# Kernel optimization log

Measured on AMD Instinct MI355X. Metric: run time of the kernel, lower is better.

The kernel has to match this reference:

```python
import jax, jax.numpy as jnp
import numpy as np

NSUB = 4  # fixed RK4 substeps per save interval (replaces diffrax adaptive stepping)


def _mlp(x, W0, b0, Wh, bh, Wo, bo, act, fact):
    h = act(W0 @ x + b0)
    for k in range(Wh.shape[0]):  # 3 stacked middle layers (static)
        h = act(Wh[k] @ h + bh[k])
    return fact(Wo @ h + bo)


def _forward(ts, ys, iW0, ib0, iWh, ibh, iWo, ibo, fW0, fb0, fWh, fbh, fWo, fbo, lW, lb):
    hid = iWo.shape[0]
    C = iW0.shape[1]  # in_size + 1 control channels

    def single(yseq):  # yseq: (T, obs)
        tys = jnp.concatenate([ts[:, None], yseq], axis=-1)  # (T, C)
        dts = ts[1:] - ts[:-1]                                # (T-1,)
        diffs = (tys[1:] - tys[:-1]) / dts[:, None]           # (T-1, C)
        # backward Hermite: deriv at t_i is backward difference, forward diff at t_0
        deriv = jnp.concatenate([diffs[:1], diffs], axis=0)   # (T, C)
        d0 = deriv[:-1]
        d1 = deriv[1:]
        c = (3.0 * diffs - 2.0 * d0 - d1) / dts[:, None]
        b = (d0 + d1 - 2.0 * diffs) / (dts * dts)[:, None]

        y0 = _mlp(tys[0], iW0, ib0, iWh, ibh, iWo, ibo, jax.nn.relu, lambda z: z)

        def vf(y):  # (hid, C)
            return _mlp(y, fW0, fb0, fWh, fbh, fWo, fbo, jax.nn.softplus, jnp.tanh).reshape(hid, C)

        def interval(y, xs):
            d0i, ci, bi, h = xs
            hs = h / NSUB

            def xdot(s):  # derivative of cubic Hermite control at local time s
                return d0i + 2.0 * ci * s + 3.0 * bi * s * s

            def f(s, yy):
                return vf(yy) @ xdot(s)

            def sub(k, yy):  # one RK4 substep
                s = k * hs
                k1 = f(s, yy)
                k2 = f(s + hs / 2, yy + hs / 2 * k1)
                k3 = f(s + hs / 2, yy + hs / 2 * k2)
                k4 = f(s + hs, yy + hs * k3)
                return yy + hs / 6 * (k1 + 2 * k2 + 2 * k3 + k4)

            y = jax.lax.fori_loop(0, NSUB, sub, y)
            return y, y

        _, ytail = jax.lax.scan(interval, y0, (d0, c, b, dts))
        ysol = jnp.concatenate([y0[None], ytail], axis=0)  # (T, hid)
        return ysol @ lW.T + lb                            # evolving_out readout

    return jax.vmap(single)(ys)


def setup_inputs() -> dict:
    key = jax.random.key(0)
    ks = jax.random.split(key, 10)
    T, B, obs, hid, width, out_size = 128, 64, 32, 64, 128, 32
    C = obs + 1
    fout = hid * C

    def lin(k, o, i):
        return jax.random.normal(k, (o, i), jnp.float32) / np.sqrt(i).astype(np.float32)

    return {
        "ts": jnp.arange(T, dtype=jnp.float32) / T,
        "ys": jax.random.normal(ks[0], (B, T, obs), jnp.float32) * 0.1,
        "iW0": lin(ks[1], width, C), "ib0": jnp.zeros((width,), jnp.float32),
        "iWh": jax.random.normal(ks[2], (3, width, width), jnp.float32) / np.sqrt(width).astype(np.float32),
        "ibh": jnp.zeros((3, width), jnp.float32),
        "iWo": lin(ks[3], hid, width), "ibo": jnp.zeros((hid,), jnp.float32),
        "fW0": lin(ks[4], width, hid), "fb0": jnp.zeros((width,), jnp.float32),
        "fWh": jax.random.normal(ks[5], (3, width, width), jnp.float32) / np.sqrt(width).astype(np.float32),
        "fbh": jnp.zeros((3, width), jnp.float32),
        "fWo": lin(ks[6], fout, width), "fbo": jnp.zeros((fout,), jnp.float32),
        "lW": lin(ks[7], out_size, hid), "lb": jnp.zeros((out_size,), jnp.float32),
    }


def reference(ts, ys, iW0, ib0, iWh, ibh, iWo, ibo, fW0, fb0, fWh, fbh, fWo, fbo, lW, lb):
    return _forward(ts, ys, iW0, ib0, iWh, ibh, iWo, ibo, fW0, fb0, fWh, fbh, fWo, fbo, lW, lb)
```

## Files before the change

kernel.cpp:

```cpp
#include <hip/hip_runtime.h>
#include <stdint.h>

#define T_N   128
#define B_N   64
#define OBS   32
#define C_N   33
#define HID   64
#define WID   128
#define FOUT  2112
#define OUTD  32
#define NSUB  4
#define NTH   1024

#define NTILE_T  132
#define NPLANES  (NTILE_T*4)
#define WS_NEED  ((size_t)NPLANES * 64 * 16)

typedef __attribute__((ext_vector_type(8))) short  bf16x8;
typedef __attribute__((ext_vector_type(4))) float  f32x4;

__device__ __forceinline__ float b2f(unsigned short u) {
    return __uint_as_float(((unsigned int)u) << 16);
}
__device__ __forceinline__ float b2f_lo(unsigned int u) {
    return __uint_as_float(u << 16);
}
__device__ __forceinline__ float b2f_hi(unsigned int u) {
    return __uint_as_float(u & 0xffff0000u);
}
__device__ __forceinline__ unsigned short f2b(float f) {
    unsigned int u = __float_as_uint(f);
    unsigned int lsb = (u >> 16) & 1u;
    u += 0x7fffu + lsb;
    return (unsigned short)(u >> 16);
}
__device__ __forceinline__ unsigned int pack2(float a, float b) {
    return ((unsigned int)f2b(a)) | (((unsigned int)f2b(b)) << 16);
}
__device__ __forceinline__ unsigned int pkhi(float a, float b) {
    return (__float_as_uint(a) >> 16) | (__float_as_uint(b) & 0xffff0000u);
}
__device__ __forceinline__ unsigned int pklo(float a, float b) {
    float la = a - __uint_as_float(__float_as_uint(a) & 0xffff0000u);
    float lb = b - __uint_as_float(__float_as_uint(b) & 0xffff0000u);
    return pack2(la, lb);
}
__device__ __forceinline__ bf16x8 u4b8(uint4 u) {
    union { uint4 a; bf16x8 b; } x; x.a = u; return x.b;
}
__device__ __forceinline__ float softplus_f(float x) {
    return fmaxf(x, 0.f) + __logf(1.f + __expf(-fabsf(x)));
}
__device__ __forceinline__ float tanh_fast(float x) {
    float e = __expf(2.f * x);
    return 1.f - 2.f / (e + 1.f);
}

struct PolBF16 {
    static __device__ __forceinline__ float ld(const void* p, int i) {
        return b2f(((const unsigned short*)p)[i]);
    }
    static __device__ __forceinline__ void ld8(const void* p, int i, float* o) {
        uint4 u = *(const uint4*)((const unsigned short*)p + i);
        o[0]=b2f_lo(u.x); o[1]=b2f_hi(u.x); o[2]=b2f_lo(u.y); o[3]=b2f_hi(u.y);
        o[4]=b2f_lo(u.z); o[5]=b2f_hi(u.z); o[6]=b2f_lo(u.w); o[7]=b2f_hi(u.w);
    }
    static __device__ __forceinline__ void st(void* p, int i, float v) {
        ((unsigned short*)p)[i] = f2b(v);
    }
};
struct PolF32 {
    static __device__ __forceinline__ float ld(const void* p, int i) {
        return ((const float*)p)[i];
    }
    static __device__ __forceinline__ void ld8(const void* p, int i, float* o) {
        const float4* q = (const float4*)((const float*)p + i);
        float4 a = q[0], b = q[1];
        o[0]=a.x; o[1]=a.y; o[2]=a.z; o[3]=a.w;
        o[4]=b.x; o[5]=b.y; o[6]=b.z; o[7]=b.w;
    }
    static __device__ __forceinline__ void st(void* p, int i, float v) {
        ((float*)p)[i] = v;
    }
};

struct __align__(16) Smem {
    uint4 whf[3][32][64];
    uint4 w0f[16][64];
    float rowp[2][FOUT];
    unsigned int hpk[2][2][64];
    unsigned int ypk[2][32];
    float y[HID];
    float yt[HID];
    float xd[C_N], d0[C_N], cc[C_N], bb[C_N];
    float fb0[WID];
    float fbh[3][WID];
    float lWt[HID*OUTD];
};

template<class P>
__device__ __forceinline__ void prep_body(const void* fWo, unsigned short* ws) {
    const int e    = blockIdx.x * NTH + threadIdx.x;
    const int p    = e >> 6;
    const int lane = e & 63;
    const int t    = p >> 2;
    const int kb   = p & 3;
    const int row  = 16*t + (lane & 15);
    const int k0   = kb*32 + ((lane >> 4) << 3);
    float v[8];
    P::ld8(fWo, row*WID + k0, v);
    uint4 u;
    u.x = pack2(v[0],v[1]); u.y = pack2(v[2],v[3]);
    u.z = pack2(v[4],v[5]); u.w = pack2(v[6],v[7]);
    ((uint4*)ws)[e] = u;
}
__global__ __launch_bounds__(NTH)
void prep_kernel(const void* ts, const void* fWo, unsigned short* ws) {
    const bool isbf = (((const unsigned short*)ts)[1] == 0x3C00);
    if (isbf) prep_body<PolBF16>(fWo, ws);
    else      prep_body<PolF32>(fWo, ws);
}

template<class P, bool COAL>
__device__ void run_cde(
    const void* ts, const void* ys, const void* iW0, const void* ib0,
    const void* iWh, const void* ibh, const void* iWo, const void* ibo,
    const void* fW0, const void* fb0, const void* fWh, const void* fbh,
    const void* fWo, const void* fbo, const void* lW, const void* lb,
    const void* wWo, void* out, Smem& S)
{
    const int tid  = threadIdx.x;
    const int b    = blockIdx.x;
    const int g16  = tid >> 4;
    const int l16  = tid & 15;
    const int r0   = g16*C_N + l16;
    const int r1   = r0 + 16;
    const int rx   = g16*C_N + 32;
    const int wv   = tid >> 6;
    const int lane = tid & 63;
    const int cidx = lane & 15;
    const int lg   = lane >> 4;
    const int pr   = wv & 7;
    const int role = wv >> 3;

    {
        const int p = tid >> 6;
        const int t = p >> 1, kb = p & 1;
        const int row = 16*t + cidx;
        const int k0  = kb*32 + lg*8;
        uint4 u;
        u.x = pack2(P::ld(fW0, row*HID + k0+0), P::ld(fW0, row*HID + k0+1));
        u.y = pack2(P::ld(fW0, row*HID + k0+2), P::ld(fW0, row*HID + k0+3));
        u.z = pack2(P::ld(fW0, row*HID + k0+4), P::ld(fW0, row*HID + k0+5));
        u.w = pack2(P::ld(fW0, row*HID + k0+6), P::ld(fW0, row*HID + k0+7));
        S.w0f[p][lane] = u;
    }
    #pragma unroll
    for (int i = 0; i < 6; ++i) {
        const int E = i*NTH + tid;
        const int p = E >> 6;
        const int ln = E & 63;
        const int l = p >> 5, rem = p & 31;
        const int t = rem >> 2, kb = rem & 3;
        const int row = 16*t + (ln & 15);
        const int k0  = kb*32 + ((ln >> 4) << 3);
        const int base = (l*WID + row)*WID + k0;
        uint4 u;
        u.x = pack2(P::ld(fWh, base+0), P::ld(fWh, base+1));
        u.y = pack2(P::ld(fWh, base+2), P::ld(fWh, base+3));
        u.z = pack2(P::ld(fWh, base+4), P::ld(fWh, base+5));
        u.w = pack2(P::ld(fWh, base+6), P::ld(fWh, base+7));
        S.whf[l][rem][ln] = u;
    }

    const float fb_r0 = P::ld(fbo, r0);
    const float fb_r1 = P::ld(fbo, r1);
    const float fb_rx = P::ld(fbo, rx);

    if (tid < WID)  S.fb0[tid] = P::ld(fb0, tid);
    if (tid < 3*WID) S.fbh[tid>>7][tid&127] = P::ld(fbh, tid);
    for (int i = tid; i < OUTD*HID; i += NTH) {
        int o = i >> 6, kk = i & 63;
        S.lWt[kk*OUTD + o] = P::ld(lW, i);
    }
    if (tid < C_N)
        S.xd[tid] = (tid == 0) ? P::ld(ts, 0) : P::ld(ys, b*T_N*OBS + (tid-1));
    __syncthreads();

    if (tid < WID) {
        float a = P::ld(ib0, tid);
        for (int k2 = 0; k2 < C_N; ++k2) a += P::ld(iW0, tid*C_N + k2) * S.xd[k2];
        S.rowp[0][tid] = fmaxf(a, 0.f);
    }
    __syncthreads();
    int pp = 0;
    for (int l = 0; l < 3; ++l) {
        if (tid < WID) {
            float a = P::ld(ibh, l*WID + tid);
            for (int k2 = 0; k2 < WID; ++k2)
                a += P::ld(iWh, (l*WID + tid)*WID + k2) * S.rowp[pp][k2];
            S.rowp[1-pp][tid] = fmaxf(a, 0.f);
        }
        __syncthreads();
        pp ^= 1;
    }
    if (tid < HID) {
        float a = P::ld(ibo, tid);
        for (int k2 = 0; k2 < WID; ++k2)
            a += P::ld(iWo, tid*WID + k2) * S.rowp[pp][k2];
        S.y[tid] = a;
    }
    __syncthreads();
    if (tid < OUTD) {
        float a = P::ld(lb, tid);
        for (int k2 = 0; k2 < HID; ++k2) a += S.lWt[k2*OUTD + tid] * S.y[k2];
        P::st(out, b*T_N*OUTD + tid, a);
    }

    #pragma unroll 1
    for (int iv = 0; iv < T_N-1; ++iv) {
        float t0 = P::ld(ts, iv), t1 = P::ld(ts, iv+1);
        float dt = t1 - t0;
        float hs = dt * (1.f/NSUB);
        if (tid < C_N) {
            float v0 = (tid==0) ? t0 : P::ld(ys, b*T_N*OBS + iv*OBS + (tid-1));
            float v1 = (tid==0) ? t1 : P::ld(ys, b*T_N*OBS + (iv+1)*OBS + (tid-1));
            float di = (v1 - v0) / dt;
            float d0v;
            if (iv == 0) d0v = di;
            else {
                float tm = P::ld(ts, iv-1);
                float vm = (tid==0) ? tm : P::ld(ys, b*T_N*OBS + (iv-1)*OBS + (tid-1));
                d0v = (v0 - vm) / (t0 - tm);
            }
            float d1v = di;
            S.d0[tid] = d0v;
            S.cc[tid] = (3.f*di - 2.f*d0v - d1v) / dt;
            S.bb[tid] = (d0v + d1v - 2.f*di) / (dt*dt);
        }
        __syncthreads();

        #pragma unroll 1
        for (int sub = 0; sub < NSUB; ++sub) {
            float s0 = sub * hs;
            float ka = 0.f, kb2 = 0.f, kc = 0.f;
            #pragma unroll 1
            for (int st = 0; st < 4; ++st) {
                float s = (st==0) ? s0 : ((st==3) ? s0+hs : s0 + 0.5f*hs);
                const float* yin = (st==0) ? S.y : S.yt;

                if (tid < 32) {
                    float v0 = yin[2*tid], v1 = yin[2*tid+1];
                    S.ypk[0][tid] = pkhi(v0, v1);
                    S.ypk[1][tid] = pklo(v0, v1);
                } else if (tid >= 64 && tid < 64 + C_N) {
                    int c = tid - 64;
                    S.xd[c] = S.d0[c] + (2.f*S.cc[c] + 3.f*S.bb[c]*s)*s;
                }
                __syncthreads();

                if (wv < 8) {
                    const int t = wv;
                    const unsigned int* hb = (cidx == 1) ? S.ypk[1] : S.ypk[0];
                    uint4 b0 = *(const uint4*)(hb + lg*4);
                    uint4 b1 = *(const uint4*)(hb + 16 + lg*4);
                    uint4 a0 = S.w0f[t*2+0][lane];
                    uint4 a1 = S.w0f[t*2+1][lane];
                    f32x4 acc = {0.f,0.f,0.f,0.f};
                    acc = __builtin_amdgcn_mfma_f32_16x16x32_bf16(
                              u4b8(a0), u4b8(b0), acc, 0, 0, 0);
                    acc = __builtin_amdgcn_mfma_f32_16x16x32_bf16(
                              u4b8(a1), u4b8(b1), acc, 0, 0, 0);
                    #pragma unroll
                    for (int r = 0; r < 4; ++r) acc[r] += __shfl_xor(acc[r], 1);
                    if (cidx == 0) {
                        const int rb = 16*t + lg*4;
                        float h0 = softplus_f(acc[0] + S.fb0[rb+0]);
                        float h1 = softplus_f(acc[1] + S.fb0[rb+1]);
                        float h2 = softplus_f(acc[2] + S.fb0[rb+2]);
                        float h3 = softplus_f(acc[3] + S.fb0[rb+3]);
                        const int o = 8*t + 2*lg;
                        S.hpk[0][0][o]   = pkhi(h0,h1);
                        S.hpk[0][0][o+1] = pkhi(h2,h3);
                        S.hpk[0][1][o]   = pklo(h0,h1);
                        S.hpk[0][1][o+1] = pklo(h2,h3);
                    }
                }
                __syncthreads();

                #pragma unroll
                for (int l = 0; l < 3; ++l) {
                    if (wv < 8) {
                        const int t = wv;
                        const unsigned int* hb = S.hpk[l & 1][(cidx==1) ? 1 : 0];
                        uint4 b0 = *(const uint4*)(hb + lg*4);
                        uint4 b1 = *(const uint4*)(hb + 16 + lg*4);
                        uint4 b2 = *(const uint4*)(hb + 32 + lg*4);
                        uint4 b3 = *(const uint4*)(hb + 48 + lg*4);
                        uint4 a0 = S.whf[l][t*4+0][lane];
                        uint4 a1 = S.whf[l][t*4+1][lane];
                        uint4 a2 = S.whf[l][t*4+2][lane];
                        uint4 a3 = S.whf[l][t*4+3][lane];
                        f32x4 acc = {0.f,0.f,0.f,0.f};
                        acc = __builtin_amdgcn_mfma_f32_16x16x32_bf16(
                                  u4b8(a0), u4b8(b0), acc, 0, 0, 0);
                        acc = __builtin_amdgcn_mfma_f32_16x16x32_bf16(
                                  u4b8(a1), u4b8(b1), acc, 0, 0, 0);
                        acc = __builtin_amdgcn_mfma_f32_16x16x32_bf16(
                                  u4b8(a2), u4b8(b2), acc, 0, 0, 0);
                        acc = __builtin_amdgcn_mfma_f32_16x16x32_bf16(
                                  u4b8(a3), u4b8(b3), acc, 0, 0, 0);
                        #pragma unroll
                        for (int r = 0; r < 4; ++r) acc[r] += __shfl_xor(acc[r], 1);
                        if (cidx == 0) {
                            const int rb = 16*t + lg*4;
                            float h0 = softplus_f(acc[0] + S.fbh[l][rb+0]);
                            float h1 = softplus_f(acc[1] + S.fbh[l][rb+1]);
                            float h2 = softplus_f(acc[2] + S.fbh[l][rb+2]);
                            float h3 = softplus_f(acc[3] + S.fbh[l][rb+3]);
                            const int o = 8*t + 2*lg;
                            unsigned int* dhi = S.hpk[1-(l&1)][0];
                            unsigned int* dlo = S.hpk[1-(l&1)][1];
                            dhi[o]   = pkhi(h0,h1);
                            dhi[o+1] = pkhi(h2,h3);
                            dlo[o]   = pklo(h0,h1);
                            dlo[o+1] = pklo(h2,h3);
                        }
                    }
                    __syncthreads();
                }

                if constexpr (COAL) {
                    const unsigned int* hb = S.hpk[1][(cidx==1) ? 1 : 0];
                    uint4 b0 = *(const uint4*)(hb + (2*role)*16 + lg*4);
                    uint4 b1 = *(const uint4*)(hb + (2*role+1)*16 + lg*4);
                    bf16x8 vb0 = u4b8(b0), vb1 = u4b8(b1);
                    const uint4* ap = (const uint4*)wWo
                                    + (pr*4 + 2*role)*64 + lane;
                    const int ntile = (pr < 4) ? 17 : 16;
                    uint4 a0 = ap[0], a1 = ap[64];
                    int t = pr;
                    #pragma unroll 1
                    for (int i = 0; i < ntile; ++i) {
                        uint4 c0 = a0, c1 = a1;
                        if (i + 1 < ntile) {
                            ap += 2048;
                            a0 = ap[0]; a1 = ap[64];
                        }
                        f32x4 acc = {0.f,0.f,0.f,0.f};
                        acc = __builtin_amdgcn_mfma_f32_16x16x32_bf16(
                                  u4b8(c0), vb0, acc, 0, 0, 0);
                        acc = __builtin_amdgcn_mfma_f32_16x16x32_bf16(
                                  u4b8(c1), vb1, acc, 0, 0, 0);
                        #pragma unroll
                        for (int r = 0; r < 4; ++r) acc[r] += __shfl_xor(acc[r], 1);
                        if (cidx == 0) {
                            float4 st4;
                            st4.x = acc[0]; st4.y = acc[1];
                            st4.z = acc[2]; st4.w = acc[3];
                            *(float4*)&S.rowp[role][16*t + lg*4] = st4;
                        }
                        t += 8;
                    }
                    __syncthreads();

                    {
                        float d0v = S.rowp[0][r0] + S.rowp[1][r0];
                        float d1v = S.rowp[0][r1] + S.rowp[1][r1];
                        float dxv = S.rowp[0][rx] + S.rowp[1][rx];
                        float v0 = tanh_fast(d0v + fb_r0) * S.xd[l16];
                        float v1 = tanh_fast(d1v + fb_r1) * S.xd[16 + l16];
                        float t2 = v0 + v1;
                        t2 += __shfl_xor(t2, 1);
                        t2 += __shfl_xor(t2, 2);
                        t2 += __shfl_xor(t2, 4);
                        t2 += __shfl_xor(t2, 8);
                        float ksum = t2 + tanh_fast(dxv + fb_rx) * S.xd[32];
                        if (l16 == 0) {
                            float yg = S.y[g16];
                            if (st == 0)      { ka = ksum;  S.yt[g16] = yg + 0.5f*hs*ksum; }
                            else if (st == 1) { kb2 = ksum; S.yt[g16] = yg + 0.5f*hs*ksum; }
                            else if (st == 2) { kc = ksum;  S.yt[g16] = yg + hs*ksum; }
                            else S.y[g16] = yg + hs*(1.f/6.f)*(ka + 2.f*kb2 + 2.f*kc + ksum);
                        }
                    }
                } else {
                    if (tid < 64) {
                        unsigned int uh = S.hpk[1][0][tid], ul = S.hpk[1][1][tid];
                        S.rowp[0][2*tid]   = b2f_lo(uh) + b2f_lo(ul);
                        S.rowp[0][2*tid+1] = b2f_hi(uh) + b2f_hi(ul);
                    }
                    __syncthreads();
                    const float* hin = S.rowp[0];
                    float a0 = 0.f, a1 = 0.f, ax = 0.f;
                    #pragma unroll 2
                    for (int j = 0; j < 16; ++j) {
                        const float4* h4 = (const float4*)(hin + j*8);
                        float4 ha = h4[0], hb2 = h4[1];
                        float w8[8];
                        P::ld8(fWo, r0*WID + j*8, w8);
                        a0 += w8[0]*ha.x + w8[1]*ha.y + w8[2]*ha.z + w8[3]*ha.w
                            + w8[4]*hb2.x + w8[5]*hb2.y + w8[6]*hb2.z + w8[7]*hb2.w;
                        P::ld8(fWo, r1*WID + j*8, w8);
                        a1 += w8[0]*ha.x + w8[1]*ha.y + w8[2]*ha.z + w8[3]*ha.w
                            + w8[4]*hb2.x + w8[5]*hb2.y + w8[6]*hb2.z + w8[7]*hb2.w;
                    }
                    {
                        float w8[8];
                        P::ld8(fWo, rx*WID + l16*8, w8);
                        const float4* h4 = (const float4*)(hin + l16*8);
                        float4 ha = h4[0], hb2 = h4[1];
                        ax = w8[0]*ha.x + w8[1]*ha.y + w8[2]*ha.z + w8[3]*ha.w
                           + w8[4]*hb2.x + w8[5]*hb2.y + w8[6]*hb2.z + w8[7]*hb2.w;
                    }
                    ax += __shfl_xor(ax, 1);
                    ax += __shfl_xor(ax, 2);
                    ax += __shfl_xor(ax, 4);
                    ax += __shfl_xor(ax, 8);
                    float v0 = tanh_fast(a0 + fb_r0) * S.xd[l16];
                    float v1 = tanh_fast(a1 + fb_r1) * S.xd[16 + l16];
                    float t2 = v0 + v1;
                    t2 += __shfl_xor(t2, 1);
                    t2 += __shfl_xor(t2, 2);
                    t2 += __shfl_xor(t2, 4);
                    t2 += __shfl_xor(t2, 8);
                    float ksum = t2 + tanh_fast(ax + fb_rx) * S.xd[32];
                    if (l16 == 0) {
                        float yg = S.y[g16];
                        if (st == 0)      { ka = ksum;  S.yt[g16] = yg + 0.5f*hs*ksum; }
                        else if (st == 1) { kb2 = ksum; S.yt[g16] = yg + 0.5f*hs*ksum; }
                        else if (st == 2) { kc = ksum;  S.yt[g16] = yg + hs*ksum; }
                        else S.y[g16] = yg + hs*(1.f/6.f)*(ka + 2.f*kb2 + 2.f*kc + ksum);
                    }
                }
                __syncthreads();
            }
        }

        if (tid < OUTD) {
            float a = P::ld(lb, tid);
            #pragma unroll 8
            for (int k2 = 0; k2 < HID; ++k2) a += S.lWt[k2*OUTD + tid] * S.y[k2];
            P::st(out, b*T_N*OUTD + (iv+1)*OUTD + tid, a);
        }
    }
}

__global__ __launch_bounds__(NTH)
void cde_kernel(const void* ts, const void* ys, const void* iW0, const void* ib0,
                const void* iWh, const void* ibh, const void* iWo, const void* ibo,
                const void* fW0, const void* fb0, const void* fWh, const void* fbh,
                const void* fWo, const void* fbo, const void* lW, const void* lb,
                const unsigned short* ws, int use_ws, void* out)
{
    __shared__ Smem S;
    const bool isbf = (((const unsigned short*)ts)[1] == 0x3C00);
    if (use_ws) {
        if (isbf)
            run_cde<PolBF16, true>(ts, ys, iW0, ib0, iWh, ibh, iWo, ibo,
                                   fW0, fb0, fWh, fbh, fWo, fbo, lW, lb,
                                   ws, out, S);
        else
            run_cde<PolF32, true>(ts, ys, iW0, ib0, iWh, ibh, iWo, ibo,
                                  fW0, fb0, fWh, fbh, fWo, fbo, lW, lb,
                                  ws, out, S);
    } else {
        if (isbf)
            run_cde<PolBF16, false>(ts, ys, iW0, ib0, iWh, ibh, iWo, ibo,
                                    fW0, fb0, fWh, fbh, fWo, fbo, lW, lb,
                                    fWo, out, S);
        else
            run_cde<PolF32, false>(ts, ys, iW0, ib0, iWh, ibh, iWo, ibo,
                                   fW0, fb0, fWh, fbh, fWo, fbo, lW, lb,
                                   fWo, out, S);
    }
}

extern "C" void kernel_launch(void* const* d_in, const int* in_sizes, int n_in,
                              void* d_out, int out_size, void* d_ws, size_t ws_size,
                              hipStream_t stream) {
    (void)in_sizes; (void)n_in; (void)out_size;
    const int use_ws = (ws_size >= WS_NEED) ? 1 : 0;
    if (use_ws) {
        const int nprep = (NPLANES * 64) / NTH;
        hipLaunchKernelGGL(prep_kernel, dim3(nprep), dim3(NTH), 0, stream,
                           d_in[0], d_in[12], (unsigned short*)d_ws);
    }
    hipLaunchKernelGGL(cde_kernel, dim3(B_N), dim3(NTH), 0, stream,
                       d_in[0], d_in[1], d_in[2], d_in[3], d_in[4], d_in[5],
                       d_in[6], d_in[7], d_in[8], d_in[9], d_in[10], d_in[11],
                       d_in[12], d_in[13], d_in[14], d_in[15],
                       (const unsigned short*)d_ws, use_ws, d_out);
}
```

Measured before the change: 16.65 ms.

## Run input and hidden MLP layers in a single wave and prefetch output weights

Wave 0 now computes the first layer and the three hidden layers by itself, eight output tiles per layer, with LDS ordering only within that wave. This removes four block-wide barriers per RK stage. The global loads of the first two output-weight tiles are issued before the remaining barrier so their latency overlaps the hidden-layer compute, and the output loop's prefetch depth grows from one tile to two. The cost is that eight times as much serial MFMA and softplus work lands on one wave while the other waves sit idle. Within the wave, a cross-lane LDS read-after-write relies on in-order execution within the wave.

New measurement: 34.95 ms. 110% more time.

```diff
diff --git a/kernel.cpp b/kernel.cpp
--- a/kernel.cpp
+++ b/kernel.cpp
@@ -249,103 +249,134 @@
                 float s = (st==0) ? s0 : ((st==3) ? s0+hs : s0 + 0.5f*hs);
                 const float* yin = (st==0) ? S.y : S.yt;
 
-                if (tid < 32) {
-                    float v0 = yin[2*tid], v1 = yin[2*tid+1];
-                    S.ypk[0][tid] = pkhi(v0, v1);
-                    S.ypk[1][tid] = pklo(v0, v1);
+                if (wv == 0) {
+                    if (lane < 32) {
+                        float v0 = yin[2*lane], v1 = yin[2*lane+1];
+                        S.ypk[0][lane] = pkhi(v0, v1);
+                        S.ypk[1][lane] = pklo(v0, v1);
+                    }
+                    {
+                        const unsigned int* yb = (cidx == 1) ? S.ypk[1]
+                                                             : S.ypk[0];
+                        uint4 b0 = *(const uint4*)(yb + lg*4);
+                        uint4 b1 = *(const uint4*)(yb + 16 + lg*4);
+                        #pragma unroll
+                        for (int half = 0; half < 2; ++half) {
+                            f32x4 acc[4];
+                            #pragma unroll
+                            for (int tt = 0; tt < 4; ++tt) {
+                                const int t = half*4 + tt;
+                                uint4 a0 = S.w0f[t*2+0][lane];
+                                uint4 a1 = S.w0f[t*2+1][lane];
+                                f32x4 z = {0.f,0.f,0.f,0.f};
+                                z = __builtin_amdgcn_mfma_f32_16x16x32_bf16(
+                                        u4b8(a0), u4b8(b0), z, 0, 0, 0);
+                                z = __builtin_amdgcn_mfma_f32_16x16x32_bf16(
+                                        u4b8(a1), u4b8(b1), z, 0, 0, 0);
+                                acc[tt] = z;
+                            }
+                            #pragma unroll
+                            for (int tt = 0; tt < 4; ++tt) {
+                                #pragma unroll
+                                for (int r = 0; r < 4; ++r)
+                                    acc[tt][r] += __shfl_xor(acc[tt][r], 1);
+                                if (cidx == 0) {
+                                    const int t = half*4 + tt;
+                                    const int rb = 16*t + lg*4;
+                                    float h0 = softplus_f(acc[tt][0] + S.fb0[rb+0]);
+                                    float h1 = softplus_f(acc[tt][1] + S.fb0[rb+1]);
+                                    float h2 = softplus_f(acc[tt][2] + S.fb0[rb+2]);
+                                    float h3 = softplus_f(acc[tt][3] + S.fb0[rb+3]);
+                                    const int o = 8*t + 2*lg;
+                                    S.hpk[0][0][o]   = pkhi(h0,h1);
+                                    S.hpk[0][0][o+1] = pkhi(h2,h3);
+                                    S.hpk[0][1][o]   = pklo(h0,h1);
+                                    S.hpk[0][1][o+1] = pklo(h2,h3);
+                                }
+                            }
+                        }
+                    }
+                    #pragma unroll
+                    for (int l = 0; l < 3; ++l) {
+                        const int ib = l & 1;
+                        const unsigned int* hb = S.hpk[ib][(cidx==1) ? 1 : 0];
+                        uint4 b0 = *(const uint4*)(hb + lg*4);
+                        uint4 b1 = *(const uint4*)(hb + 16 + lg*4);
+                        uint4 b2 = *(const uint4*)(hb + 32 + lg*4);
+                        uint4 b3 = *(const uint4*)(hb + 48 + lg*4);
+                        #pragma unroll
+                        for (int half = 0; half < 2; ++half) {
+                            f32x4 acc[4];
+                            #pragma unroll
+                            for (int tt = 0; tt < 4; ++tt) {
+                                const int t = half*4 + tt;
+                                uint4 a0 = S.whf[l][t*4+0][lane];
+                                uint4 a1 = S.whf[l][t*4+1][lane];
+                                uint4 a2 = S.whf[l][t*4+2][lane];
+                                uint4 a3 = S.whf[l][t*4+3][lane];
+                                f32x4 z = {0.f,0.f,0.f,0.f};
+                                z = __builtin_amdgcn_mfma_f32_16x16x32_bf16(
+                                        u4b8(a0), u4b8(b0), z, 0, 0, 0);
+                                z = __builtin_amdgcn_mfma_f32_16x16x32_bf16(
+                                        u4b8(a1), u4b8(b1), z, 0, 0, 0);
+                                z = __builtin_amdgcn_mfma_f32_16x16x32_bf16(
+                                        u4b8(a2), u4b8(b2), z, 0, 0, 0);
+                                z = __builtin_amdgcn_mfma_f32_16x16x32_bf16(
+                                        u4b8(a3), u4b8(b3), z, 0, 0, 0);
+                                acc[tt] = z;
+                            }
+                            #pragma unroll
+                            for (int tt = 0; tt < 4; ++tt) {
+                                #pragma unroll
+                                for (int r = 0; r < 4; ++r)
+                                    acc[tt][r] += __shfl_xor(acc[tt][r], 1);
+                                if (cidx == 0) {
+                                    const int t = half*4 + tt;
+                                    const int rb = 16*t + lg*4;
+                                    float h0 = softplus_f(acc[tt][0] + S.fbh[l][rb+0]);
+                                    float h1 = softplus_f(acc[tt][1] + S.fbh[l][rb+1]);
+                                    float h2 = softplus_f(acc[tt][2] + S.fbh[l][rb+2]);
+                                    float h3 = softplus_f(acc[tt][3] + S.fbh[l][rb+3]);
+                                    const int o = 8*t + 2*lg;
+                                    unsigned int* dhi = S.hpk[1-ib][0];
+                                    unsigned int* dlo = S.hpk[1-ib][1];
+                                    dhi[o]   = pkhi(h0,h1);
+                                    dhi[o+1] = pkhi(h2,h3);
+                                    dlo[o]   = pklo(h0,h1);
+                                    dlo[o+1] = pklo(h2,h3);
+                                }
+                            }
+                        }
+                    }
                 } else if (tid >= 64 && tid < 64 + C_N) {
                     int c = tid - 64;
                     S.xd[c] = S.d0[c] + (2.f*S.cc[c] + 3.f*S.bb[c]*s)*s;
                 }
-                __syncthreads();
-
-                if (wv < 8) {
-                    const int t = wv;
-                    const unsigned int* hb = (cidx == 1) ? S.ypk[1] : S.ypk[0];
-                    uint4 b0 = *(const uint4*)(hb + lg*4);
-                    uint4 b1 = *(const uint4*)(hb + 16 + lg*4);
-                    uint4 a0 = S.w0f[t*2+0][lane];
-                    uint4 a1 = S.w0f[t*2+1][lane];
-                    f32x4 acc = {0.f,0.f,0.f,0.f};
-                    acc = __builtin_amdgcn_mfma_f32_16x16x32_bf16(
-                              u4b8(a0), u4b8(b0), acc, 0, 0, 0);
-                    acc = __builtin_amdgcn_mfma_f32_16x16x32_bf16(
-                              u4b8(a1), u4b8(b1), acc, 0, 0, 0);
-                    #pragma unroll
-                    for (int r = 0; r < 4; ++r) acc[r] += __shfl_xor(acc[r], 1);
-                    if (cidx == 0) {
-                        const int rb = 16*t + lg*4;
-                        float h0 = softplus_f(acc[0] + S.fb0[rb+0]);
-                        float h1 = softplus_f(acc[1] + S.fb0[rb+1]);
-                        float h2 = softplus_f(acc[2] + S.fb0[rb+2]);
-                        float h3 = softplus_f(acc[3] + S.fb0[rb+3]);
-                        const int o = 8*t + 2*lg;
-                        S.hpk[0][0][o]   = pkhi(h0,h1);
-                        S.hpk[0][0][o+1] = pkhi(h2,h3);
-                        S.hpk[0][1][o]   = pklo(h0,h1);
-                        S.hpk[0][1][o+1] = pklo(h2,h3);
-                    }
+
+                const uint4* ap = (const uint4*)wWo + (pr*4 + 2*role)*64 + lane;
+                uint4 pa0, pa1, pa2, pa3;
+                const uint4* ap2 = ap + 2048;
+                if constexpr (COAL) {
+                    pa0 = ap[0]; pa1 = ap[64];
+                    pa2 = ap2[0]; pa3 = ap2[64];
                 }
                 __syncthreads();
-
-                #pragma unroll
-                for (int l = 0; l < 3; ++l) {
-                    if (wv < 8) {
-                        const int t = wv;
-                        const unsigned int* hb = S.hpk[l & 1][(cidx==1) ? 1 : 0];
-                        uint4 b0 = *(const uint4*)(hb + lg*4);
-                        uint4 b1 = *(const uint4*)(hb + 16 + lg*4);
-                        uint4 b2 = *(const uint4*)(hb + 32 + lg*4);
-                        uint4 b3 = *(const uint4*)(hb + 48 + lg*4);
-                        uint4 a0 = S.whf[l][t*4+0][lane];
-                        uint4 a1 = S.whf[l][t*4+1][lane];
-                        uint4 a2 = S.whf[l][t*4+2][lane];
-                        uint4 a3 = S.whf[l][t*4+3][lane];
-                        f32x4 acc = {0.f,0.f,0.f,0.f};
-                        acc = __builtin_amdgcn_mfma_f32_16x16x32_bf16(
-                                  u4b8(a0), u4b8(b0), acc, 0, 0, 0);
-                        acc = __builtin_amdgcn_mfma_f32_16x16x32_bf16(
-                                  u4b8(a1), u4b8(b1), acc, 0, 0, 0);
-                        acc = __builtin_amdgcn_mfma_f32_16x16x32_bf16(
-                                  u4b8(a2), u4b8(b2), acc, 0, 0, 0);
-                        acc = __builtin_amdgcn_mfma_f32_16x16x32_bf16(
-                                  u4b8(a3), u4b8(b3), acc, 0, 0, 0);
-                        #pragma unroll
-                        for (int r = 0; r < 4; ++r) acc[r] += __shfl_xor(acc[r], 1);
-                        if (cidx == 0) {
-                            const int rb = 16*t + lg*4;
-                            float h0 = softplus_f(acc[0] + S.fbh[l][rb+0]);
-                            float h1 = softplus_f(acc[1] + S.fbh[l][rb+1]);
-                            float h2 = softplus_f(acc[2] + S.fbh[l][rb+2]);
-                            float h3 = softplus_f(acc[3] + S.fbh[l][rb+3]);
-                            const int o = 8*t + 2*lg;
-                            unsigned int* dhi = S.hpk[1-(l&1)][0];
-                            unsigned int* dlo = S.hpk[1-(l&1)][1];
-                            dhi[o]   = pkhi(h0,h1);
-                            dhi[o+1] = pkhi(h2,h3);
-                            dlo[o]   = pklo(h0,h1);
-                            dlo[o+1] = pklo(h2,h3);
-                        }
-                    }
-                    __syncthreads();
-                }
 
                 if constexpr (COAL) {
                     const unsigned int* hb = S.hpk[1][(cidx==1) ? 1 : 0];
                     uint4 b0 = *(const uint4*)(hb + (2*role)*16 + lg*4);
                     uint4 b1 = *(const uint4*)(hb + (2*role+1)*16 + lg*4);
                     bf16x8 vb0 = u4b8(b0), vb1 = u4b8(b1);
-                    const uint4* ap = (const uint4*)wWo
-                                    + (pr*4 + 2*role)*64 + lane;
                     const int ntile = (pr < 4) ? 17 : 16;
-                    uint4 a0 = ap[0], a1 = ap[64];
+                    uint4 a0 = pa0, a1 = pa1, a2 = pa2, a3 = pa3;
                     int t = pr;
                     #pragma unroll 1
                     for (int i = 0; i < ntile; ++i) {
                         uint4 c0 = a0, c1 = a1;
-                        if (i + 1 < ntile) {
-                            ap += 2048;
-                            a0 = ap[0]; a1 = ap[64];
+                        a0 = a2; a1 = a3;
+                        if (i + 2 < ntile) {
+                            ap2 += 2048;
+                            a2 = ap2[0]; a3 = ap2[64];
                         }
                         f32x4 acc = {0.f,0.f,0.f,0.f};
                         acc = __builtin_amdgcn_mfma_f32_16x16x32_bf16(
```
